# Performance work log

Measured on AMD Instinct MI355X. Metric: run time of the kernel, lower is better.

Reference implementation:

```python
import jax, jax.numpy as jnp
import numpy as np

P = 10          # num_patches
EPS = 1e-20
ALPHAS = dict(stretch=1.0, E=1.0, G=1.0, skew=1.0, total_area=1.0, total_area_mult=1.0)
ALPHA_MC = 1.0
ALPHA_DISTORT = 1.0


def setup_inputs() -> dict:
    key = jax.random.key(0)
    k1, k2, k3, k4 = jax.random.split(key, 4)
    B, N, M = 8, 8192, 2500
    pc_gt = jax.random.normal(k1, (B, N, 3), dtype=jnp.float32)
    pc_pred = jax.random.normal(k2, (B, M, 3), dtype=jnp.float32)
    # first fundamental form (E, F, G); ensure E*G - F^2 > 0 so sqrt is smooth
    u = jax.random.uniform(k3, (B, M, 3), dtype=jnp.float32)
    fff = u * 0.5 + jnp.array([1.0, 0.0, 1.0], dtype=jnp.float32)
    A_gt = jax.random.uniform(k4, (B,), dtype=jnp.float32)
    return {"pc_gt": pc_gt, "pc_pred": pc_pred, "fff": fff, "A_gt": A_gt}


def _forward(pc_gt, pc_pred, fff, A_gt):
    B, M, _ = pc_pred.shape
    spp = M // P

    # ---- Chamfer distance via dense (B, M, N) distance matrix + argmin ----
    diff = pc_pred[:, :, None, :] - pc_gt[:, None, :, :]          # (B, M, N, 3)
    distm = jnp.sqrt(jnp.sum(diff * diff, axis=3))                # (B, M, N)
    inds_p2gt = jnp.argmin(distm, axis=2)                         # (B, M)
    inds_gt2p = jnp.argmin(distm, axis=1)                         # (B, N)
    pc_gt_reg = jnp.take_along_axis(pc_gt, inds_p2gt[..., None], axis=1)   # (B, M, 3)
    pc_p_reg = jnp.take_along_axis(pc_pred, inds_gt2p[..., None], axis=1)  # (B, N, 3)
    d_p2gt = jnp.sum((pc_pred - pc_gt_reg) ** 2, axis=2)
    d_gt2p = jnp.sum((pc_gt - pc_p_reg) ** 2, axis=2)
    L_chd = d_p2gt.mean() + d_gt2p.mean()

    # ---- FFF-based losses ----
    EFG = jnp.transpose(fff.reshape(B, P, spp, 3), (3, 0, 1, 2))  # (3, B, P, spp)
    E, F, G = EFG[0], EFG[1], EFG[2]

    # metric consistency between consecutive frame pairs
    Eh = E.reshape(B // 2, 2, P, spp)
    Fh = F.reshape(B // 2, 2, P, spp)
    Gh = G.reshape(B // 2, 2, P, spp)
    L_mc = ((Eh[:, 0] - Eh[:, 1]) ** 2
            + 2.0 * (Fh[:, 0] - Fh[:, 1]) ** 2
            + (Gh[:, 0] - Gh[:, 1]) ** 2).mean()

    # scaled isometry (collapse) losses
    A2 = jnp.maximum(E * G - F * F, 0.0)                          # (B, P, spp)
    A = jnp.sqrt(A2)
    inv = 1.0 / (A2 + EPS)
    L_stretch = (((E - G) ** 2) * inv).mean() * ALPHAS['stretch']
    L_E = (((E - E.mean()) ** 2) * inv).mean() * ALPHAS['E']
    L_G = (((G - G.mean()) ** 2) * inv).mean() * ALPHAS['G']
    L_F = ((F * F) * inv).mean() * ALPHAS['skew']

    # overlap / total-area loss
    A_tot = A.mean(axis=2).sum(axis=1)                            # (B,)
    L_olap = (jnp.maximum(0.0, A_tot - A_gt * ALPHAS['total_area_mult']) ** 2).mean() * ALPHAS['total_area']

    loss_sciso = L_F + L_E + L_G + L_stretch + L_olap
    loss_tot = L_chd + ALPHA_MC * L_mc + ALPHA_DISTORT * loss_sciso
    return loss_tot


def reference(pc_gt, pc_pred, fff, A_gt):
    return _forward(pc_gt, pc_pred, fff, A_gt)
```

## Files before the change

kernel.cpp:

```cpp
#include <hip/hip_runtime.h>

#define B_   8
#define N_   8192
#define M_   2500
#define SPP_ 250
#define EPS_ 1e-20f
#define BIGF 1e30f

#define NB_CH   320
#define NB_FFF  79
#define NB_K1   (NB_CH + NB_FFF)

#define NB_RG2P 256
#define NB_RP2  79
#define NB_K2   (NB_RG2P + NB_RP2)

#define WS_P2GT 0
#define WS_GT2P 160000
#define WS_ACC  487680
#define WS_RED  487700
#define WS_CNT  488035
#define A_E    0
#define A_G    1
#define A_MC   2
#define A_ST   3
#define A_F2I  4
#define A_E2I  5
#define A_EI   6
#define A_G2I  7
#define A_GI   8
#define A_I    9
#define A_AB   10
#define RO_G2P 0
#define RO_P2  256

typedef __attribute__((ext_vector_type(8))) short short8_t;
typedef __attribute__((ext_vector_type(4))) float float4_t;

__device__ __forceinline__ unsigned pack_bf2(float lo, float hi) {
    unsigned a = __float_as_uint(lo);
    unsigned b = __float_as_uint(hi);
    a = (a + 0x7FFFu + ((a >> 16) & 1u)) >> 16;
    b = (b + 0x7FFFu + ((b >> 16) & 1u)) & 0xFFFF0000u;
    return a | b;
}
__device__ __forceinline__ short bf16s(float x) {
    unsigned a = __float_as_uint(x);
    return (short)((a + 0x7FFFu + ((a >> 16) & 1u)) >> 16);
}
__device__ __forceinline__ float wave_sum64(float v) {
    #pragma unroll
    for (int o = 32; o > 0; o >>= 1) v += __shfl_down(v, o, 64);
    return v;
}
__device__ __forceinline__ float block_sum256(float v, volatile float* red4) {
    v = wave_sum64(v);
    int wid = threadIdx.x >> 6, lane = threadIdx.x & 63;
    if (lane == 0) red4[wid] = v;
    __syncthreads();
    float r = 0.f;
    if (threadIdx.x == 0) r = red4[0] + red4[1] + red4[2] + red4[3];
    __syncthreads();
    return r;
}
__device__ __forceinline__ void min4(float4_t& c, const float4_t d) {
    c.x = fminf(c.x, d.x); c.y = fminf(c.y, d.y);
    c.z = fminf(c.z, d.z); c.w = fminf(c.w, d.w);
}
__device__ __forceinline__ void quad_min4(float4_t& c) {
    #pragma unroll
    for (int m = 1; m < 16; m <<= 1) {
        c.x = fminf(c.x, __shfl_xor(c.x, m, 64));
        c.y = fminf(c.y, __shfl_xor(c.y, m, 64));
        c.z = fminf(c.z, __shfl_xor(c.z, m, 64));
        c.w = fminf(c.w, __shfl_xor(c.w, m, 64));
    }
}

__global__ void __launch_bounds__(256, 2) k1_main(
        const float* __restrict__ gt, const float* __restrict__ pred,
        const float* __restrict__ fff, float* __restrict__ ws) {
    __shared__ uint4 spts[1024];
    __shared__ __align__(16) float saux[516];
    __shared__ float scol[4][1024];
    const int bid = blockIdx.x;
    const int tid = threadIdx.x;
    const int lane = tid & 63;
    const int w    = tid >> 6;
    const int quad = lane >> 4;
    const int l15  = lane & 15;
    float* acc = ws + WS_ACC;

    if (bid == 0 && tid == 0) ((unsigned*)(ws + WS_CNT))[0] = 0u;

    if (bid < NB_CH) {
        const int z = bid / 40;
        const int rem = bid % 40;
        const int b = rem / 5;
        const int mblk = rem % 5;
        const float* apts = pred + (size_t)b * M_ * 3;
        const float* bpts = gt + ((size_t)b * N_ + (size_t)z * 1024) * 3;
        const int alim = M_;
        const int abase = mblk * 512;
        float* dstR = ws + WS_P2GT + (size_t)z * 20000 + b * M_;
        float* dstC = ws + WS_GT2P + (size_t)mblk * 65536 + b * N_ + z * 1024;

        for (int i = tid; i < 1024; i += 256) {
            const float* q3 = bpts + i * 3;
            float x = q3[0], y = q3[1], zc = q3[2];
            float n2 = x * x + y * y + zc * zc;
            uint4 q;
            q.x = pack_bf2(-2.f * x, -2.f * y);
            q.y = pack_bf2(-2.f * zc, n2);
            q.z = q.x; q.w = q.y;
            spts[i] = q;
        }

        short8_t af[8];
        #pragma unroll
        for (int t = 0; t < 8; ++t) af[t] = (short8_t){0,0,0,0,0,0,0,0};
        if (lane < 16) {
            #pragma unroll
            for (int t = 0; t < 8; ++t) {
                int m = abase + w * 128 + t * 16 + l15;
                int c = m < alim ? m : alim - 1;
                float x = apts[c*3+0], y = apts[c*3+1], zc = apts[c*3+2];
                af[t][0] = bf16s(x); af[t][1] = bf16s(y); af[t][2] = bf16s(zc);
                af[t][3] = (short)0x3F80;
                saux[w * 128 + t * 16 + l15] = x*x + y*y + zc*zc;
            }
        }
        __syncthreads();

        const float4_t* bp = (const float4_t*)saux;
        float4_t bias[8], c[8];
        #pragma unroll
        for (int t = 0; t < 8; ++t) {
            bias[t] = bp[w * 32 + t * 4 + quad];
            c[t] = (float4_t){BIGF, BIGF, BIGF, BIGF};
        }

        const uint4* bptr = spts + l15;
        #pragma unroll 2
        for (int i = 0; i < 64; ++i) {
            short8_t bf = __builtin_bit_cast(short8_t, bptr[i * 16]);
            float cmA = BIGF, cmB = BIGF;
            #pragma unroll
            for (int t = 0; t < 8; ++t) {
                float4_t d = __builtin_amdgcn_mfma_f32_16x16x32_bf16(
                                 af[t], bf, bias[t], 0, 0, 0);
                min4(c[t], d);
                float m0 = fminf(fminf(d.x, d.y), fminf(d.z, d.w));
                if (t & 1) cmB = fminf(cmB, m0); else cmA = fminf(cmA, m0);
            }
            float cm = fminf(cmA, cmB);
            cm = fminf(cm, __shfl_xor(cm, 16, 64));
            cm = fminf(cm, __shfl_xor(cm, 32, 64));
            if (lane < 16) scol[w][i * 16 + l15] = cm;
        }

        #pragma unroll
        for (int t = 0; t < 8; ++t) {
            quad_min4(c[t]);
            c[t].x = fmaxf(c[t].x, 0.f); c[t].y = fmaxf(c[t].y, 0.f);
            c[t].z = fmaxf(c[t].z, 0.f); c[t].w = fmaxf(c[t].w, 0.f);
        }
        if (l15 == 0) {
            #pragma unroll
            for (int t = 0; t < 8; ++t) {
                int m0 = abase + w * 128 + t * 16 + quad * 4;
                if (m0 < alim)
                    *(float4_t*)(dstR + m0) = c[t];
            }
        }

        __syncthreads();
        #pragma unroll
        for (int j = tid; j < 1024; j += 256) {
            float v = fminf(fminf(scol[0][j], scol[1][j]),
                            fminf(scol[2][j], scol[3][j]));
            dstC[j] = fmaxf(v, 0.f);
        }
    } else {
        const int kb = bid - NB_CH;
        const int i  = kb * 256 + tid;
        volatile float* red4 = saux + 512;
        float* sA = saux;
        if (tid < B_) sA[tid] = 0.f;
        __syncthreads();

        float vE=0.f,vG=0.f,vMC=0.f,vST=0.f,vF2=0.f,vE2=0.f,vEI=0.f,
              vG2=0.f,vGI=0.f,vI=0.f;
        if (i < B_ * M_) {
            const int b = i / M_;
            const int m = i - b * M_;
            const float* f = fff + (size_t)i * 3;
            float E = f[0], F = f[1], G = f[2];
            float A2  = fmaxf(E * G - F * F, 0.f);
            float inv = 1.f / (A2 + EPS_);
            vE = E; vG = G;
            vST = (E - G) * (E - G) * inv;
            vF2 = F * F * inv;
            vE2 = E * E * inv; vEI = E * inv;
            vG2 = G * G * inv; vGI = G * inv;
            vI  = inv;
            atomicAdd(&sA[b], sqrtf(A2));
            if ((b & 1) == 0) {
                const float* f2 = fff + ((size_t)(b + 1) * M_ + m) * 3;
                float dE = E - f2[0], dF = F - f2[1], dG = G - f2[2];
                vMC = dE * dE + 2.f * dF * dF + dG * dG;
            }
        }
        float r;
        r = block_sum256(vE,  red4); if (tid==0) atomicAdd(&acc[A_E],   r);
        r = block_sum256(vG,  red4); if (tid==0) atomicAdd(&acc[A_G],   r);
        r = block_sum256(vMC, red4); if (tid==0) atomicAdd(&acc[A_MC],  r);
        r = block_sum256(vST, red4); if (tid==0) atomicAdd(&acc[A_ST],  r);
        r = block_sum256(vF2, red4); if (tid==0) atomicAdd(&acc[A_F2I], r);
        r = block_sum256(vE2, red4); if (tid==0) atomicAdd(&acc[A_E2I], r);
        r = block_sum256(vEI, red4); if (tid==0) atomicAdd(&acc[A_EI],  r);
        r = block_sum256(vG2, red4); if (tid==0) atomicAdd(&acc[A_G2I], r);
        r = block_sum256(vGI, red4); if (tid==0) atomicAdd(&acc[A_GI],  r);
        r = block_sum256(vI,  red4); if (tid==0) atomicAdd(&acc[A_I],   r);
        __syncthreads();
        if (tid < B_ && sA[tid] != 0.f) atomicAdd(&acc[A_AB + tid], sA[tid]);
    }
}

__global__ void __launch_bounds__(256) k2_reduce(
        const float* __restrict__ fff, const float* __restrict__ A_gt,
        float* __restrict__ ws, float* __restrict__ out) {
    __shared__ float red4[4];
    const int bid = blockIdx.x;
    const int tid = threadIdx.x;
    float* redp = ws + WS_RED;
    float* acc  = ws + WS_ACC;

    if (bid < NB_RG2P) {
        const int o = bid * 256 + tid;
        const float* src = ws + WS_GT2P + o;
        float m = src[0];
        #pragma unroll
        for (int zz = 1; zz < 5; ++zz) m = fminf(m, src[zz * 65536]);
        float r = block_sum256(m, red4);
        if (tid == 0) redp[RO_G2P + bid] = r;
    } else {
        const int kb = bid - NB_RG2P;
        const int o = kb * 256 + tid;
        float s = 0.f;
        if (o < 20000) {
            const float* src = ws + WS_P2GT + o;
            float m = src[0];
            #pragma unroll
            for (int zz = 1; zz < 8; ++zz) m = fminf(m, src[zz * 20000]);
            s = m;
        }
        float r = block_sum256(s, red4);
        if (tid == 0) redp[RO_P2 + kb] = r;
    }

    __syncthreads();
    if (tid == 0) __threadfence();
    __syncthreads();
    __shared__ unsigned old_s;
    if (tid == 0)
        old_s = __hip_atomic_fetch_add((unsigned*)(ws + WS_CNT), 1u,
                                       __ATOMIC_ACQ_REL, __HIP_MEMORY_SCOPE_AGENT);
    __syncthreads();
    if (old_s == (unsigned)(NB_K2 - 1)) {
        float v;
        v = redp[RO_G2P + tid];
        float sGT2P = block_sum256(v, red4);
        v = (tid < 79) ? redp[RO_P2 + tid] : 0.f;
        float sP2GT = block_sum256(v, red4);
        if (tid == 0) {
            float a[18];
            #pragma unroll
            for (int k = 0; k < 18; ++k)
                a[k] = __hip_atomic_load(&acc[k], __ATOMIC_RELAXED,
                                         __HIP_MEMORY_SCOPE_AGENT);
            const float inv20k = 1.f / 20000.f;
            float mE = a[A_E] * inv20k, mG = a[A_G] * inv20k;
            float L_E = (a[A_E2I] - 2.f*mE*a[A_EI] + mE*mE*a[A_I]) * inv20k;
            float L_G = (a[A_G2I] - 2.f*mG*a[A_GI] + mG*mG*a[A_I]) * inv20k;
            float L_sc = L_E + L_G + (a[A_ST] + a[A_F2I]) * inv20k;
            float L_mc = a[A_MC] * (1.f / 10000.f);
            float L_chd = sP2GT * inv20k + sGT2P * (1.f / 65536.f);
            float L_olap = 0.f;
            #pragma unroll
            for (int b = 0; b < B_; ++b) {
                float At = a[A_AB + b] * (1.f / (float)SPP_);
                float d  = fmaxf(0.f, At - A_gt[b]);
                L_olap += d * d;
            }
            L_olap *= (1.f / (float)B_);
            out[0] = L_chd + L_mc + L_sc + L_olap;
        }
    }
}

extern "C" void kernel_launch(void* const* d_in, const int* in_sizes, int n_in,
                              void* d_out, int out_size, void* d_ws, size_t ws_size,
                              hipStream_t stream) {
    const float* pc_gt   = (const float*)d_in[0];
    const float* pc_pred = (const float*)d_in[1];
    const float* fff     = (const float*)d_in[2];
    const float* A_gt    = (const float*)d_in[3];
    float* ws  = (float*)d_ws;
    float* out = (float*)d_out;

    hipMemsetAsync(ws + WS_ACC, 0, 20 * sizeof(float), stream);
    k1_main  <<<NB_K1, 256, 0, stream>>>(pc_gt, pc_pred, fff, ws);
    k2_reduce<<<NB_K2, 256, 0, stream>>>(fff, A_gt, ws, out);
}
```

Before: 104.0 us.

## Split Chamfer tiles finer, merge minima with atomicMin, batch MFMA pairs

Halves the ground-truth points per block and doubles the Chamfer block count, so the grid fills more of the GPU. Per-tile minima are now merged in place with integer atomicMin on non-negative float bits, into a workspace pre-filled with a large value by an extra memset. That replaces the partial-minimum arrays and shrinks the second kernel to a plain sum reduction finished with atomics. The inner loop issues two MFMAs per step, uses v_min3, and keeps per-quad column minima in shared memory instead of cross-lane shuffles. The trade-offs are more global atomics and one extra memset launch.

```diff
diff --git a/kernel.cpp b/kernel.cpp
--- a/kernel.cpp
+++ b/kernel.cpp
@@ -7,19 +7,18 @@
 #define EPS_ 1e-20f
 #define BIGF 1e30f
 
-#define NB_CH   320
+#define NB_CH   640
 #define NB_FFF  79
 #define NB_K1   (NB_CH + NB_FFF)
 
-#define NB_RG2P 256
-#define NB_RP2  79
-#define NB_K2   (NB_RG2P + NB_RP2)
-
-#define WS_P2GT 0
-#define WS_GT2P 160000
-#define WS_ACC  487680
-#define WS_RED  487700
-#define WS_CNT  488035
+#define NB_SG   64
+#define NB_SP   20
+#define NB_K2   (NB_SG + NB_SP)
+
+#define WS_P2M  0
+#define WS_G2M  20000
+#define WS_ACC  85536
+#define WS_CNT  (WS_ACC + 20)
 #define A_E    0
 #define A_G    1
 #define A_MC   2
@@ -31,8 +30,8 @@
 #define A_GI   8
 #define A_I    9
 #define A_AB   10
-#define RO_G2P 0
-#define RO_P2  256
+#define A_SP   18
+#define A_SG   19
 
 typedef __attribute__((ext_vector_type(8))) short short8_t;
 typedef __attribute__((ext_vector_type(4))) float float4_t;
@@ -48,6 +47,11 @@
     unsigned a = __float_as_uint(x);
     return (short)((a + 0x7FFFu + ((a >> 16) & 1u)) >> 16);
 }
+__device__ __forceinline__ float min3f(float a, float b, float c) {
+    float r;
+    asm("v_min3_f32 %0, %1, %2, %3" : "=v"(r) : "v"(a), "v"(b), "v"(c));
+    return r;
+}
 __device__ __forceinline__ float wave_sum64(float v) {
     #pragma unroll
     for (int o = 32; o > 0; o >>= 1) v += __shfl_down(v, o, 64);
@@ -62,10 +66,6 @@
     if (threadIdx.x == 0) r = red4[0] + red4[1] + red4[2] + red4[3];
     __syncthreads();
     return r;
-}
-__device__ __forceinline__ void min4(float4_t& c, const float4_t d) {
-    c.x = fminf(c.x, d.x); c.y = fminf(c.y, d.y);
-    c.z = fminf(c.z, d.z); c.w = fminf(c.w, d.w);
 }
 __device__ __forceinline__ void quad_min4(float4_t& c) {
     #pragma unroll
@@ -80,9 +80,9 @@
 __global__ void __launch_bounds__(256, 2) k1_main(
         const float* __restrict__ gt, const float* __restrict__ pred,
         const float* __restrict__ fff, float* __restrict__ ws) {
-    __shared__ uint4 spts[1024];
+    __shared__ uint4 spts[512];
     __shared__ __align__(16) float saux[516];
-    __shared__ float scol[4][1024];
+    __shared__ float scol[4][4][520];
     const int bid = blockIdx.x;
     const int tid = threadIdx.x;
     const int lane = tid & 63;
@@ -91,21 +91,18 @@
     const int l15  = lane & 15;
     float* acc = ws + WS_ACC;
 
-    if (bid == 0 && tid == 0) ((unsigned*)(ws + WS_CNT))[0] = 0u;
-
     if (bid < NB_CH) {
         const int z = bid / 40;
         const int rem = bid % 40;
         const int b = rem / 5;
         const int mblk = rem % 5;
         const float* apts = pred + (size_t)b * M_ * 3;
-        const float* bpts = gt + ((size_t)b * N_ + (size_t)z * 1024) * 3;
-        const int alim = M_;
+        const float* bpts = gt + ((size_t)b * N_ + (size_t)z * 512) * 3;
         const int abase = mblk * 512;
-        float* dstR = ws + WS_P2GT + (size_t)z * 20000 + b * M_;
-        float* dstC = ws + WS_GT2P + (size_t)mblk * 65536 + b * N_ + z * 1024;
-
-        for (int i = tid; i < 1024; i += 256) {
+        float* dstR = ws + WS_P2M + (size_t)b * M_;
+        float* dstC = ws + WS_G2M + (size_t)b * N_ + z * 512;
+
+        for (int i = tid; i < 512; i += 256) {
             const float* q3 = bpts + i * 3;
             float x = q3[0], y = q3[1], zc = q3[2];
             float n2 = x * x + y * y + zc * zc;
@@ -123,7 +120,7 @@
             #pragma unroll
             for (int t = 0; t < 8; ++t) {
                 int m = abase + w * 128 + t * 16 + l15;
-                int c = m < alim ? m : alim - 1;
+                int c = m < M_ ? m : M_ - 1;
                 float x = apts[c*3+0], y = apts[c*3+1], zc = apts[c*3+2];
                 af[t][0] = bf16s(x); af[t][1] = bf16s(y); af[t][2] = bf16s(zc);
                 af[t][3] = (short)0x3F80;
@@ -142,44 +139,57 @@
 
         const uint4* bptr = spts + l15;
         #pragma unroll 2
-        for (int i = 0; i < 64; ++i) {
-            short8_t bf = __builtin_bit_cast(short8_t, bptr[i * 16]);
-            float cmA = BIGF, cmB = BIGF;
+        for (int ip = 0; ip < 16; ++ip) {
+            short8_t bf0 = __builtin_bit_cast(short8_t, bptr[(2*ip+0) * 16]);
+            short8_t bf1 = __builtin_bit_cast(short8_t, bptr[(2*ip+1) * 16]);
+            float4_t d0[8], d1[8];
+            #pragma unroll
+            for (int t = 0; t < 8; ++t)
+                d0[t] = __builtin_amdgcn_mfma_f32_16x16x32_bf16(af[t], bf0, bias[t], 0, 0, 0);
+            #pragma unroll
+            for (int t = 0; t < 8; ++t)
+                d1[t] = __builtin_amdgcn_mfma_f32_16x16x32_bf16(af[t], bf1, bias[t], 0, 0, 0);
+            float cA0 = BIGF, cB0 = BIGF, cA1 = BIGF, cB1 = BIGF;
             #pragma unroll
             for (int t = 0; t < 8; ++t) {
-                float4_t d = __builtin_amdgcn_mfma_f32_16x16x32_bf16(
-                                 af[t], bf, bias[t], 0, 0, 0);
-                min4(c[t], d);
-                float m0 = fminf(fminf(d.x, d.y), fminf(d.z, d.w));
-                if (t & 1) cmB = fminf(cmB, m0); else cmA = fminf(cmA, m0);
+                c[t].x = min3f(c[t].x, d0[t].x, d1[t].x);
+                c[t].y = min3f(c[t].y, d0[t].y, d1[t].y);
+                c[t].z = min3f(c[t].z, d0[t].z, d1[t].z);
+                c[t].w = min3f(c[t].w, d0[t].w, d1[t].w);
+                float m0 = min3f(d0[t].x, d0[t].y, d0[t].z);
+                float m1 = min3f(d1[t].x, d1[t].y, d1[t].z);
+                if (t & 1) { cB0 = min3f(cB0, m0, d0[t].w); cB1 = min3f(cB1, m1, d1[t].w); }
+                else       { cA0 = min3f(cA0, m0, d0[t].w); cA1 = min3f(cA1, m1, d1[t].w); }
             }
-            float cm = fminf(cmA, cmB);
-            cm = fminf(cm, __shfl_xor(cm, 16, 64));
-            cm = fminf(cm, __shfl_xor(cm, 32, 64));
-            if (lane < 16) scol[w][i * 16 + l15] = cm;
+            scol[w][quad][(2*ip+0)*16 + l15] = fminf(cA0, cB0);
+            scol[w][quad][(2*ip+1)*16 + l15] = fminf(cA1, cB1);
         }
 
         #pragma unroll
         for (int t = 0; t < 8; ++t) {
             quad_min4(c[t]);
-            c[t].x = fmaxf(c[t].x, 0.f); c[t].y = fmaxf(c[t].y, 0.f);
-            c[t].z = fmaxf(c[t].z, 0.f); c[t].w = fmaxf(c[t].w, 0.f);
-        }
-        if (l15 == 0) {
-            #pragma unroll
-            for (int t = 0; t < 8; ++t) {
+            if (l15 == 0) {
                 int m0 = abase + w * 128 + t * 16 + quad * 4;
-                if (m0 < alim)
-                    *(float4_t*)(dstR + m0) = c[t];
+                if (m0 < M_) {
+                    atomicMin((int*)(dstR + m0 + 0), (int)__float_as_uint(fmaxf(c[t].x, 0.f)));
+                    atomicMin((int*)(dstR + m0 + 1), (int)__float_as_uint(fmaxf(c[t].y, 0.f)));
+                    atomicMin((int*)(dstR + m0 + 2), (int)__float_as_uint(fmaxf(c[t].z, 0.f)));
+                    atomicMin((int*)(dstR + m0 + 3), (int)__float_as_uint(fmaxf(c[t].w, 0.f)));
+                }
             }
         }
 
         __syncthreads();
         #pragma unroll
-        for (int j = tid; j < 1024; j += 256) {
-            float v = fminf(fminf(scol[0][j], scol[1][j]),
-                            fminf(scol[2][j], scol[3][j]));
-            dstC[j] = fmaxf(v, 0.f);
+        for (int rr = 0; rr < 2; ++rr) {
+            int j = rr * 256 + tid;
+            float v = BIGF;
+            #pragma unroll
+            for (int w2 = 0; w2 < 4; ++w2)
+                #pragma unroll
+                for (int q = 0; q < 4; ++q)
+                    v = fminf(v, scol[w2][q][j]);
+            atomicMin((int*)(dstC + j), (int)__float_as_uint(fmaxf(v, 0.f)));
         }
     } else {
         const int kb = bid - NB_CH;
@@ -233,30 +243,25 @@
     __shared__ float red4[4];
     const int bid = blockIdx.x;
     const int tid = threadIdx.x;
-    float* redp = ws + WS_RED;
-    float* acc  = ws + WS_ACC;
-
-    if (bid < NB_RG2P) {
-        const int o = bid * 256 + tid;
-        const float* src = ws + WS_GT2P + o;
-        float m = src[0];
-        #pragma unroll
-        for (int zz = 1; zz < 5; ++zz) m = fminf(m, src[zz * 65536]);
-        float r = block_sum256(m, red4);
-        if (tid == 0) redp[RO_G2P + bid] = r;
+    float* acc = ws + WS_ACC;
+
+    if (bid < NB_SG) {
+        const float* src = ws + WS_G2M + (size_t)bid * 1024;
+        float s = 0.f;
+        #pragma unroll
+        for (int j = 0; j < 4; ++j) s += src[tid + j * 256];
+        float r = block_sum256(s, red4);
+        if (tid == 0) atomicAdd(&acc[A_SG], r);
     } else {
-        const int kb = bid - NB_RG2P;
-        const int o = kb * 256 + tid;
+        const int kb = bid - NB_SG;
         float s = 0.f;
-        if (o < 20000) {
-            const float* src = ws + WS_P2GT + o;
-            float m = src[0];
-            #pragma unroll
-            for (int zz = 1; zz < 8; ++zz) m = fminf(m, src[zz * 20000]);
-            s = m;
+        #pragma unroll
+        for (int j = 0; j < 4; ++j) {
+            int o = kb * 1024 + tid + j * 256;
+            if (o < 20000) s += ws[WS_P2M + o];
         }
         float r = block_sum256(s, red4);
-        if (tid == 0) redp[RO_P2 + kb] = r;
+        if (tid == 0) atomicAdd(&acc[A_SP], r);
     }
 
     __syncthreads();
@@ -267,35 +272,28 @@
         old_s = __hip_atomic_fetch_add((unsigned*)(ws + WS_CNT), 1u,
                                        __ATOMIC_ACQ_REL, __HIP_MEMORY_SCOPE_AGENT);
     __syncthreads();
-    if (old_s == (unsigned)(NB_K2 - 1)) {
-        float v;
-        v = redp[RO_G2P + tid];
-        float sGT2P = block_sum256(v, red4);
-        v = (tid < 79) ? redp[RO_P2 + tid] : 0.f;
-        float sP2GT = block_sum256(v, red4);
-        if (tid == 0) {
-            float a[18];
-            #pragma unroll
-            for (int k = 0; k < 18; ++k)
-                a[k] = __hip_atomic_load(&acc[k], __ATOMIC_RELAXED,
-                                         __HIP_MEMORY_SCOPE_AGENT);
-            const float inv20k = 1.f / 20000.f;
-            float mE = a[A_E] * inv20k, mG = a[A_G] * inv20k;
-            float L_E = (a[A_E2I] - 2.f*mE*a[A_EI] + mE*mE*a[A_I]) * inv20k;
-            float L_G = (a[A_G2I] - 2.f*mG*a[A_GI] + mG*mG*a[A_I]) * inv20k;
-            float L_sc = L_E + L_G + (a[A_ST] + a[A_F2I]) * inv20k;
-            float L_mc = a[A_MC] * (1.f / 10000.f);
-            float L_chd = sP2GT * inv20k + sGT2P * (1.f / 65536.f);
-            float L_olap = 0.f;
-            #pragma unroll
-            for (int b = 0; b < B_; ++b) {
-                float At = a[A_AB + b] * (1.f / (float)SPP_);
-                float d  = fmaxf(0.f, At - A_gt[b]);
-                L_olap += d * d;
-            }
-            L_olap *= (1.f / (float)B_);
-            out[0] = L_chd + L_mc + L_sc + L_olap;
-        }
+    if (old_s == (unsigned)(NB_K2 - 1) && tid == 0) {
+        float a[20];
+        #pragma unroll
+        for (int k = 0; k < 20; ++k)
+            a[k] = __hip_atomic_load(&acc[k], __ATOMIC_RELAXED,
+                                     __HIP_MEMORY_SCOPE_AGENT);
+        const float inv20k = 1.f / 20000.f;
+        float mE = a[A_E] * inv20k, mG = a[A_G] * inv20k;
+        float L_E = (a[A_E2I] - 2.f*mE*a[A_EI] + mE*mE*a[A_I]) * inv20k;
+        float L_G = (a[A_G2I] - 2.f*mG*a[A_GI] + mG*mG*a[A_I]) * inv20k;
+        float L_sc = L_E + L_G + (a[A_ST] + a[A_F2I]) * inv20k;
+        float L_mc = a[A_MC] * (1.f / 10000.f);
+        float L_chd = a[A_SP] * inv20k + a[A_SG] * (1.f / 65536.f);
+        float L_olap = 0.f;
+        #pragma unroll
+        for (int b = 0; b < B_; ++b) {
+            float At = a[A_AB + b] * (1.f / (float)SPP_);
+            float d  = fmaxf(0.f, At - A_gt[b]);
+            L_olap += d * d;
+        }
+        L_olap *= (1.f / (float)B_);
+        out[0] = L_chd + L_mc + L_sc + L_olap;
     }
 }
 
@@ -309,7 +307,8 @@
     float* ws  = (float*)d_ws;
     float* out = (float*)d_out;
 
-    hipMemsetAsync(ws + WS_ACC, 0, 20 * sizeof(float), stream);
+    hipMemsetAsync(ws, 0x7F, (size_t)WS_ACC * sizeof(float), stream);
+    hipMemsetAsync(ws + WS_ACC, 0, 21 * sizeof(float), stream);
     k1_main  <<<NB_K1, 256, 0, stream>>>(pc_gt, pc_pred, fff, ws);
     k2_reduce<<<NB_K2, 256, 0, stream>>>(fff, A_gt, ws, out);
 }
```

After: 91.47 us. 12.1% less time.
